# Optimization experiments

Hardware: AMD Instinct MI355X
Metric: run time of the kernel (lower is better)

## Reference

```python
import jax, jax.numpy as jnp
import numpy as np

H = 16          # num heads
HD = 88         # head dim = 1408 / 16
IMG = 336
PATCH = 14
THETA = 10000.0
IDX = IMG // PATCH          # 24 patches per side
SEQ = IDX * IDX + 1         # 576 patches + 1 CLS slot = 577


def _vision_rope_cos_sin():
    # Faithful to HF Llama4VisionRotaryEmbedding (rope_type='llama4', complex64):
    # 2D rope over (x, y) patch coordinates; CLS token gets zero rotation.
    img_idx = np.arange(IDX * IDX, dtype=np.int64).reshape(-1, 1)
    img_idx = np.concatenate([img_idx, img_idx[:1]], axis=0)
    img_idx[-1, -1] = -2  # CLS token marker
    fx = img_idx % IDX
    fy = img_idx // IDX
    freq_dim = HD // 2  # 44
    rope_freq = 1.0 / (THETA ** (np.arange(0, freq_dim, 2)[: freq_dim // 2].astype(np.float64) / freq_dim))
    freqs_x = np.repeat((fx + 1)[..., None] * rope_freq[None, None, :], 2, axis=-1)
    freqs_y = np.repeat((fy + 1)[..., None] * rope_freq[None, None, :], 2, axis=-1)
    freqs = np.concatenate([freqs_x, freqs_y], axis=-1)[..., ::2]  # [SEQ, 1, HD//2]
    freqs = np.where(img_idx.reshape(-1, 1, 1) < 0, 0.0, freqs)
    return jnp.asarray(np.cos(freqs), jnp.float32), jnp.asarray(np.sin(freqs), jnp.float32)


def _apply_rope(x, cos, sin):
    # x: [B, S, H, HD]; treat last dim as HD//2 complex pairs, rotate by e^{i*freq}
    xr = x.reshape(*x.shape[:-1], HD // 2, 2)
    a, b = xr[..., 0], xr[..., 1]               # [B, S, H, HD//2]
    out_r = a * cos - b * sin                   # cos/sin [S,1,HD//2] broadcast over B,H
    out_i = a * sin + b * cos
    return jnp.stack([out_r, out_i], axis=-1).reshape(x.shape)


def setup_inputs() -> dict:
    key = jax.random.key(0)
    ks = jax.random.split(key, 9)
    D = H * HD  # 1408
    B, S = 32, SEQ
    s = 0.02
    return {
        "hidden_states": jax.random.normal(ks[0], (B, S, D), jnp.float32),
        "wq": jax.random.normal(ks[1], (D, D), jnp.float32) * s,
        "bq": jax.random.normal(ks[2], (D,), jnp.float32) * s,
        "wk": jax.random.normal(ks[3], (D, D), jnp.float32) * s,
        "bk": jax.random.normal(ks[4], (D,), jnp.float32) * s,
        "wv": jax.random.normal(ks[5], (D, D), jnp.float32) * s,
        "bv": jax.random.normal(ks[6], (D,), jnp.float32) * s,
        "wo": jax.random.normal(ks[7], (D, D), jnp.float32) * s,
        "bo": jax.random.normal(ks[8], (D,), jnp.float32) * s,
    }


def reference(hidden_states, wq, bq, wk, bk, wv, bv, wo, bo):
    B, S, D = hidden_states.shape
    cos, sin = _vision_rope_cos_sin()
    # QKV projections (torch Linear convention: y = x @ W.T + b)
    q = (hidden_states @ wq.T + bq).reshape(B, S, H, HD)
    k = (hidden_states @ wk.T + bk).reshape(B, S, H, HD)
    v = (hidden_states @ wv.T + bv).reshape(B, S, H, HD)
    q = _apply_rope(q, cos, sin)
    k = _apply_rope(k, cos, sin)
    # Full (non-causal) self-attention
    scores = jnp.einsum('bqhd,bkhd->bhqk', q, k) * (HD ** -0.5)
    probs = jax.nn.softmax(scores, axis=-1)
    attn = jnp.einsum('bhqk,bkhd->bqhd', probs, v).reshape(B, S, D)
    return attn @ wo.T + bo
```

## Files before the change

kernel.cpp:

```cpp
#include <hip/hip_runtime.h>
#include <hip/hip_bf16.h>
#include <cstdint>
#include <cstddef>

#define NHEADS 16
#define HDIM   88
#define SEQLEN 577
#define NBATCH 32
#define DMODEL 1408
#define MROWS  (NBATCH * SEQLEN)
#define MTILES 145
#define MPAD   (MTILES * 128)
#define SP     592
#define SPT    592
#define DP     96
#define NFREQ  44
#define NBH    (NBATCH * NHEADS)

typedef __attribute__((ext_vector_type(8))) short short8;
typedef __attribute__((ext_vector_type(4))) float floatx4;

__device__ __forceinline__ unsigned short f2bf(float f) {
    union { float f; unsigned u; } v; v.f = f;
    unsigned u = v.u;
    u += 0x7fffu + ((u >> 16) & 1u);
    return (unsigned short)(u >> 16);
}

__device__ __forceinline__ void gload_lds16(const void* g, void* lds) {
    __builtin_amdgcn_global_load_lds(
        (__attribute__((address_space(1))) unsigned int*)g,
        (__attribute__((address_space(3))) unsigned int*)lds, 16, 0, 0);
}

__global__ void l4v_rope_table(float* __restrict__ cos_t, float* __restrict__ sin_t) {
    int idx = blockIdx.x * blockDim.x + threadIdx.x;
    if (idx >= SEQLEN * NFREQ) return;
    int s = idx / NFREQ, j = idx % NFREQ;
    float ang = 0.0f;
    if (s != SEQLEN - 1) {
        int coord = (j < 22) ? (s % 24) : (s / 24);
        int i = (j < 22) ? j : j - 22;
        float rf = __expf(-(2.0f * (float)i / 44.0f) * 9.21034037197618f);
        ang = (float)(coord + 1) * rf;
    }
    cos_t[idx] = cosf(ang);
    sin_t[idx] = sinf(ang);
}

__global__ void l4v_cvt_bf16(const float* __restrict__ in, unsigned short* __restrict__ out, int n) {
    int i = (blockIdx.x * blockDim.x + threadIdx.x) * 4;
    if (i + 3 < n) {
        float4 f = *(const float4*)(in + i);
        ushort4 o;
        o.x = f2bf(f.x); o.y = f2bf(f.y); o.z = f2bf(f.z); o.w = f2bf(f.w);
        *(ushort4*)(out + i) = o;
    } else {
        for (; i < n; i++) out[i] = f2bf(in[i]);
    }
}

__global__ __launch_bounds__(256, 3)
void l4v_gemm_qkv(const unsigned short* __restrict__ A,
                  const unsigned short* __restrict__ Wq,
                  const unsigned short* __restrict__ Wk,
                  const unsigned short* __restrict__ Wv,
                  const float* __restrict__ Bq,
                  const float* __restrict__ Bk,
                  const float* __restrict__ Bv,
                  const float* __restrict__ cos_t,
                  const float* __restrict__ sin_t,
                  unsigned short* __restrict__ Oq,
                  unsigned short* __restrict__ Ok,
                  unsigned short* __restrict__ OvT)
{
    __shared__ __align__(16) unsigned short a_sm[128 * 32];
    __shared__ __align__(16) unsigned short b_sm[128 * 32];

    const int tid  = threadIdx.x;
    const int lane = tid & 63;
    const int w    = tid >> 6;
    const int quad = lane >> 4;
    const int c    = lane & 15;
    const int wr   = w >> 1;
    const int wc   = w & 1;
    const int sel  = blockIdx.x % 3;
    const int n0   = (blockIdx.x / 3) * 128;
    const int m0   = blockIdx.y * 128;

    const unsigned short* Bw = (sel == 0) ? Wq : (sel == 1) ? Wk : Wv;
    const float* bias        = (sel == 0) ? Bq : (sel == 1) ? Bk : Bv;

    floatx4 acc[4][4];
#pragma unroll
    for (int i = 0; i < 4; i++)
#pragma unroll
        for (int j = 0; j < 4; j++) acc[i][j] = (floatx4)0.0f;

    const int chunk0 = w * 128 + lane;
    const int chunk1 = w * 128 + 64 + lane;
    const int r0 = chunk0 >> 2, ch0 = chunk0 & 3;
    const int r1 = chunk1 >> 2, ch1 = chunk1 & 3;
    const unsigned short* Ab = A  + (size_t)m0 * DMODEL;
    const unsigned short* Bb = Bw + (size_t)n0 * DMODEL;

    for (int k0 = 0; k0 < DMODEL; k0 += 32) {
        gload_lds16(Ab + (size_t)r0 * DMODEL + k0 + ch0 * 8, a_sm + (w * 128) * 8);
        gload_lds16(Ab + (size_t)r1 * DMODEL + k0 + ch1 * 8, a_sm + (w * 128 + 64) * 8);
        gload_lds16(Bb + (size_t)r0 * DMODEL + k0 + ch0 * 8, b_sm + (w * 128) * 8);
        gload_lds16(Bb + (size_t)r1 * DMODEL + k0 + ch1 * 8, b_sm + (w * 128 + 64) * 8);
        __syncthreads();
        short8 af[4], bfr[4];
#pragma unroll
        for (int mt = 0; mt < 4; mt++)
            af[mt] = *(const short8*)(a_sm + (wr * 64 + mt * 16 + c) * 32 + quad * 8);
#pragma unroll
        for (int nt = 0; nt < 4; nt++)
            bfr[nt] = *(const short8*)(b_sm + (wc * 64 + nt * 16 + c) * 32 + quad * 8);
#pragma unroll
        for (int mt = 0; mt < 4; mt++)
#pragma unroll
            for (int nt = 0; nt < 4; nt++)
                acc[mt][nt] = __builtin_amdgcn_mfma_f32_16x16x32_bf16(af[mt], bfr[nt], acc[mt][nt], 0, 0, 0);
        __syncthreads();
    }

    if (sel < 2) {
        unsigned short* outp = (sel == 0) ? Oq : Ok;
#pragma unroll
        for (int mt = 0; mt < 4; mt++) {
            int mbase = m0 + wr * 64 + mt * 16 + quad * 4;
#pragma unroll
            for (int nt = 0; nt < 4; nt++) {
                int n = n0 + wc * 64 + nt * 16 + c;
                float bi = bias[n];
                int h = n / HDIM, d = n % HDIM, j = d >> 1;
#pragma unroll
                for (int r = 0; r < 4; r++) {
                    int m = mbase + r;
                    int b = m / SEQLEN;
                    int s = m - b * SEQLEN;
                    float v = acc[mt][nt][r] + bi;
                    float pv = __shfl_xor(v, 1);
                    float cs = cos_t[s * NFREQ + j];
                    float sn = sin_t[s * NFREQ + j];
                    float outv = ((d & 1) == 0) ? (v * cs - pv * sn) : (pv * sn + v * cs);
                    if (m < MROWS)
                        outp[((size_t)(b * NHEADS + h) * SP + s) * DP + d] = f2bf(outv);
                }
            }
        }
    } else {
#pragma unroll
        for (int mt = 0; mt < 4; mt++) {
            int mbase = m0 + wr * 64 + mt * 16 + quad * 4;
#pragma unroll
            for (int nt = 0; nt < 4; nt++) {
                int n = n0 + wc * 64 + nt * 16 + c;
                float bi = bias[n];
                int h = n / HDIM, d = n % HDIM;
#pragma unroll
                for (int r = 0; r < 4; r++) {
                    int m = mbase + r;
                    if (m < MROWS) {
                        int b = m / SEQLEN;
                        int s = m - b * SEQLEN;
                        OvT[((size_t)((b * NHEADS + h) * DP + d)) * SPT + s] =
                            f2bf(acc[mt][nt][r] + bi);
                    }
                }
            }
        }
    }
}

__global__ __launch_bounds__(256, 3)
void l4v_gemm_out(const unsigned short* __restrict__ A,
                  const unsigned short* __restrict__ Bw,
                  const float* __restrict__ bias,
                  float* __restrict__ out_f32)
{
    __shared__ __align__(16) unsigned short a_sm[128 * 32];
    __shared__ __align__(16) unsigned short b_sm[128 * 32];

    const int tid  = threadIdx.x;
    const int lane = tid & 63;
    const int w    = tid >> 6;
    const int quad = lane >> 4;
    const int c    = lane & 15;
    const int wr   = w >> 1;
    const int wc   = w & 1;
    const int m0   = blockIdx.y * 128;
    const int n0   = blockIdx.x * 128;

    floatx4 acc[4][4];
#pragma unroll
    for (int i = 0; i < 4; i++)
#pragma unroll
        for (int j = 0; j < 4; j++) acc[i][j] = (floatx4)0.0f;

    const int chunk0 = w * 128 + lane;
    const int chunk1 = w * 128 + 64 + lane;
    const int r0 = chunk0 >> 2, ch0 = chunk0 & 3;
    const int r1 = chunk1 >> 2, ch1 = chunk1 & 3;
    const unsigned short* Ab = A  + (size_t)m0 * DMODEL;
    const unsigned short* Bb = Bw + (size_t)n0 * DMODEL;

    for (int k0 = 0; k0 < DMODEL; k0 += 32) {
        gload_lds16(Ab + (size_t)r0 * DMODEL + k0 + ch0 * 8, a_sm + (w * 128) * 8);
        gload_lds16(Ab + (size_t)r1 * DMODEL + k0 + ch1 * 8, a_sm + (w * 128 + 64) * 8);
        gload_lds16(Bb + (size_t)r0 * DMODEL + k0 + ch0 * 8, b_sm + (w * 128) * 8);
        gload_lds16(Bb + (size_t)r1 * DMODEL + k0 + ch1 * 8, b_sm + (w * 128 + 64) * 8);
        __syncthreads();
        short8 af[4], bfr[4];
#pragma unroll
        for (int mt = 0; mt < 4; mt++)
            af[mt] = *(const short8*)(a_sm + (wr * 64 + mt * 16 + c) * 32 + quad * 8);
#pragma unroll
        for (int nt = 0; nt < 4; nt++)
            bfr[nt] = *(const short8*)(b_sm + (wc * 64 + nt * 16 + c) * 32 + quad * 8);
#pragma unroll
        for (int mt = 0; mt < 4; mt++)
#pragma unroll
            for (int nt = 0; nt < 4; nt++)
                acc[mt][nt] = __builtin_amdgcn_mfma_f32_16x16x32_bf16(af[mt], bfr[nt], acc[mt][nt], 0, 0, 0);
        __syncthreads();
    }

#pragma unroll
    for (int mt = 0; mt < 4; mt++) {
        int mbase = m0 + wr * 64 + mt * 16 + quad * 4;
#pragma unroll
        for (int nt = 0; nt < 4; nt++) {
            int n = n0 + wc * 64 + nt * 16 + c;
            float bi = bias[n];
#pragma unroll
            for (int r = 0; r < 4; r++) {
                int m = mbase + r;
                if (m < MROWS) out_f32[(size_t)m * DMODEL + n] = acc[mt][nt][r] + bi;
            }
        }
    }
}

__global__ __launch_bounds__(256, 4)
void l4v_attn(const unsigned short* __restrict__ Q,
              const unsigned short* __restrict__ K,
              const unsigned short* __restrict__ VT,
              unsigned short* __restrict__ Obuf)
{
    __shared__ __align__(16) unsigned short k_sm[64 * 104];
    __shared__ __align__(16) unsigned short v_sm[96 * 72];
    __shared__ __align__(16) unsigned short p_sm[4][16 * 72];

    const int tid  = threadIdx.x;
    const int lane = tid & 63;
    const int w    = tid >> 6;
    const int quad = lane >> 4;
    const int c    = lane & 15;
    const int bh   = blockIdx.y;
    const int b    = bh >> 4, h = bh & 15;
    const size_t base  = (size_t)bh * SP * DP;
    const size_t baseT = (size_t)bh * DP * SPT;
    const float sl2e = 0.10660035817780522f * 1.4426950408889634f;

    for (int qi = 0; qi < 5; qi++) {
        const int qt = blockIdx.x * 5 + qi;

        int qrow = qt * 64 + w * 16 + c;
        if (qrow > SP - 1) qrow = SP - 1;
        short8 aq[3];
#pragma unroll
        for (int ks = 0; ks < 3; ks++)
            aq[ks] = *(const short8*)(Q + base + (size_t)qrow * DP + ks * 32 + quad * 8);

        float m_run[4], l_run[4];
        floatx4 o_acc[6];
#pragma unroll
        for (int r = 0; r < 4; r++) { m_run[r] = -INFINITY; l_run[r] = 0.0f; }
#pragma unroll
        for (int i = 0; i < 6; i++) o_acc[i] = (floatx4)0.0f;

        for (int kt = 0; kt < 10; kt++) {
#pragma unroll
            for (int i = 0; i < 3; i++) {
                int cc = tid + i * 256;
                int krr = cc / 12, kcol = cc - krr * 12;
                int krow = kt * 64 + krr;
                if (krow > SP - 1) krow = SP - 1;
                float4 kd = *(const float4*)(K + base + (size_t)krow * DP + kcol * 8);
                *(float4*)(k_sm + krr * 104 + kcol * 8) = kd;

                int vrow = cc >> 3, vcol = cc & 7;
                int scol = kt * 64 + vcol * 8;
                if (scol > SPT - 8) scol = SPT - 8;
                float4 vd = *(const float4*)(VT + baseT + (size_t)vrow * SPT + scol);
                *(float4*)(v_sm + vrow * 72 + vcol * 8) = vd;
            }
            __syncthreads();

            floatx4 sc[4];
#pragma unroll
            for (int nt = 0; nt < 4; nt++) {
                sc[nt] = (floatx4)0.0f;
#pragma unroll
                for (int ks = 0; ks < 3; ks++) {
                    short8 bk = *(const short8*)(k_sm + (nt * 16 + c) * 104 + ks * 32 + quad * 8);
                    sc[nt] = __builtin_amdgcn_mfma_f32_16x16x32_bf16(aq[ks], bk, sc[nt], 0, 0, 0);
                }
            }

            float t[4][4];
#pragma unroll
            for (int nt = 0; nt < 4; nt++) {
                int skcol = kt * 64 + nt * 16 + c;
                bool valid = (skcol < SEQLEN);
#pragma unroll
                for (int r = 0; r < 4; r++)
                    t[nt][r] = valid ? sc[nt][r] * sl2e : -INFINITY;
            }

            float mnew[4], alpha[4];
#pragma unroll
            for (int r = 0; r < 4; r++) {
                float v = fmaxf(fmaxf(t[0][r], t[1][r]), fmaxf(t[2][r], t[3][r]));
#pragma unroll
                for (int off = 1; off < 16; off <<= 1) v = fmaxf(v, __shfl_xor(v, off));
                mnew[r] = fmaxf(m_run[r], v);
                alpha[r] = exp2f(m_run[r] - mnew[r]);
                m_run[r] = mnew[r];
            }

            float p[4][4];
#pragma unroll
            for (int nt = 0; nt < 4; nt++)
#pragma unroll
                for (int r = 0; r < 4; r++)
                    p[nt][r] = exp2f(t[nt][r] - mnew[r]);

#pragma unroll
            for (int r = 0; r < 4; r++) {
                float sm = p[0][r] + p[1][r] + p[2][r] + p[3][r];
#pragma unroll
                for (int off = 1; off < 16; off <<= 1) sm += __shfl_xor(sm, off);
                l_run[r] = l_run[r] * alpha[r] + sm;
            }

#pragma unroll
            for (int nt = 0; nt < 4; nt++)
#pragma unroll
                for (int r = 0; r < 4; r++)
                    p_sm[w][(quad * 4 + r) * 72 + nt * 16 + c] = f2bf(p[nt][r]);

#pragma unroll
            for (int i = 0; i < 6; i++)
#pragma unroll
                for (int r = 0; r < 4; r++)
                    o_acc[i][r] *= alpha[r];

#pragma unroll
            for (int kp = 0; kp < 2; kp++) {
                short8 ap = *(const short8*)(&p_sm[w][c * 72 + kp * 32 + quad * 8]);
#pragma unroll
                for (int d2 = 0; d2 < 6; d2++) {
                    short8 bv = *(const short8*)(v_sm + (d2 * 16 + c) * 72 + kp * 32 + quad * 8);
                    o_acc[d2] = __builtin_amdgcn_mfma_f32_16x16x32_bf16(ap, bv, o_acc[d2], 0, 0, 0);
                }
            }
            __syncthreads();
        }

#pragma unroll
        for (int r = 0; r < 4; r++) {
            int sq = qt * 64 + w * 16 + quad * 4 + r;
            float il = 1.0f / l_run[r];
            if (sq < SEQLEN) {
                size_t rowoff = ((size_t)b * SEQLEN + sq) * DMODEL + h * HDIM;
#pragma unroll
                for (int d2 = 0; d2 < 6; d2++) {
                    int d = d2 * 16 + c;
                    if (d < HDIM) Obuf[rowoff + d] = f2bf(o_acc[d2][r] * il);
                }
            }
        }
    }
}

extern "C" void kernel_launch(void* const* d_in, const int* in_sizes, int n_in,
                              void* d_out, int out_size, void* d_ws, size_t ws_size,
                              hipStream_t stream)
{
    const float* hs = (const float*)d_in[0];
    const float* wq = (const float*)d_in[1];
    const float* bq = (const float*)d_in[2];
    const float* wk = (const float*)d_in[3];
    const float* bk = (const float*)d_in[4];
    const float* wv = (const float*)d_in[5];
    const float* bv = (const float*)d_in[6];
    const float* wo = (const float*)d_in[7];
    const float* bo = (const float*)d_in[8];
    float* out = (float*)d_out;

    char* ws = (char*)d_ws;
    size_t off = 0;
    auto alloc = [&](size_t bytes) -> char* {
        char* p = ws + off;
        off += (bytes + 255) & ~(size_t)255;
        return p;
    };

    unsigned short* hs_bf = (unsigned short*)alloc((size_t)MPAD * DMODEL * 2);
    unsigned short* wq_bf = (unsigned short*)alloc((size_t)DMODEL * DMODEL * 2);
    unsigned short* wk_bf = (unsigned short*)alloc((size_t)DMODEL * DMODEL * 2);
    unsigned short* wv_bf = (unsigned short*)alloc((size_t)DMODEL * DMODEL * 2);
    unsigned short* wo_bf = (unsigned short*)alloc((size_t)DMODEL * DMODEL * 2);
    unsigned short* qb    = (unsigned short*)alloc((size_t)NBH * SP * DP * 2);
    unsigned short* kb    = (unsigned short*)alloc((size_t)NBH * SP * DP * 2);
    unsigned short* vt    = (unsigned short*)alloc((size_t)NBH * DP * SPT * 2);
    float* cos_t = (float*)alloc((size_t)SEQLEN * NFREQ * 4);
    float* sin_t = (float*)alloc((size_t)SEQLEN * NFREQ * 4);
    unsigned short* attn_bf = hs_bf;

    if (off > ws_size) return;

    l4v_rope_table<<<dim3((SEQLEN * NFREQ + 255) / 256), dim3(256), 0, stream>>>(cos_t, sin_t);

    const int nhs = MROWS * DMODEL;
    l4v_cvt_bf16<<<dim3(nhs / 4 / 256), dim3(256), 0, stream>>>(hs, hs_bf, nhs);
    const int nw = DMODEL * DMODEL;
    l4v_cvt_bf16<<<dim3(nw / 4 / 256), dim3(256), 0, stream>>>(wq, wq_bf, nw);
    l4v_cvt_bf16<<<dim3(nw / 4 / 256), dim3(256), 0, stream>>>(wk, wk_bf, nw);
    l4v_cvt_bf16<<<dim3(nw / 4 / 256), dim3(256), 0, stream>>>(wv, wv_bf, nw);
    l4v_cvt_bf16<<<dim3(nw / 4 / 256), dim3(256), 0, stream>>>(wo, wo_bf, nw);

    l4v_gemm_qkv<<<dim3(33, MTILES), dim3(256), 0, stream>>>(
        hs_bf, wq_bf, wk_bf, wv_bf, bq, bk, bv, cos_t, sin_t, qb, kb, vt);

    l4v_attn<<<dim3(2, NBH), dim3(256), 0, stream>>>(qb, kb, vt, attn_bf);

    l4v_gemm_out<<<dim3(DMODEL / 128, MTILES), dim3(256), 0, stream>>>(attn_bf, wo_bf, bo, out);
}
```

Before: 1.043 ms.

## Double K-step per sync, swizzle GEMM block order, merge weight casts

Both GEMMs now load two 32-wide K slices into two LDS buffers per iteration, so each pair of barriers covers 64 K elements instead of 32. Blocks are launched on a 1D grid and remapped so groups of 29 M-tiles sweep all N-tiles together, which is meant to improve L2 reuse of the activation rows. The four weight bf16 conversions are merged into one launch. The change doubles LDS use per block, which may lower occupancy under launch_bounds(256,3). It also relies on MTILES=145 being exactly 5*29.

```diff
diff --git a/kernel.cpp b/kernel.cpp
--- a/kernel.cpp
+++ b/kernel.cpp
@@ -58,6 +58,22 @@
     } else {
         for (; i < n; i++) out[i] = f2bf(in[i]);
     }
+}
+
+__global__ void l4v_cvt_w4(const float* __restrict__ w0, const float* __restrict__ w1,
+                           const float* __restrict__ w2, const float* __restrict__ w3,
+                           unsigned short* __restrict__ o0, unsigned short* __restrict__ o1,
+                           unsigned short* __restrict__ o2, unsigned short* __restrict__ o3,
+                           int nw) {
+    int i = (blockIdx.x * blockDim.x + threadIdx.x) * 4;
+    int which = i / nw;
+    int local = i - which * nw;
+    const float* src = (which == 0) ? w0 : (which == 1) ? w1 : (which == 2) ? w2 : w3;
+    unsigned short* dst = (which == 0) ? o0 : (which == 1) ? o1 : (which == 2) ? o2 : o3;
+    float4 f = *(const float4*)(src + local);
+    ushort4 o;
+    o.x = f2bf(f.x); o.y = f2bf(f.y); o.z = f2bf(f.z); o.w = f2bf(f.w);
+    *(ushort4*)(dst + local) = o;
 }
 
 __global__ __launch_bounds__(256, 3)
@@ -74,8 +90,8 @@
                   unsigned short* __restrict__ Ok,
                   unsigned short* __restrict__ OvT)
 {
-    __shared__ __align__(16) unsigned short a_sm[128 * 32];
-    __shared__ __align__(16) unsigned short b_sm[128 * 32];
+    __shared__ __align__(16) unsigned short a_sm[2][128 * 32];
+    __shared__ __align__(16) unsigned short b_sm[2][128 * 32];
 
     const int tid  = threadIdx.x;
     const int lane = tid & 63;
@@ -84,9 +100,15 @@
     const int c    = lane & 15;
     const int wr   = w >> 1;
     const int wc   = w & 1;
-    const int sel  = blockIdx.x % 3;
-    const int n0   = (blockIdx.x / 3) * 128;
-    const int m0   = blockIdx.y * 128;
+
+    const int bid  = blockIdx.x;
+    const int SG   = 29 * 33;
+    const int sg   = bid / SG;
+    const int rr   = bid - sg * SG;
+    const int m0   = (sg * 29 + (rr % 29)) * 128;
+    const int xsel = rr / 29;
+    const int sel  = xsel / 11;
+    const int n0   = (xsel - sel * 11) * 128;
 
     const unsigned short* Bw = (sel == 0) ? Wq : (sel == 1) ? Wk : Wv;
     const float* bias        = (sel == 0) ? Bq : (sel == 1) ? Bk : Bv;
@@ -104,24 +126,33 @@
     const unsigned short* Ab = A  + (size_t)m0 * DMODEL;
     const unsigned short* Bb = Bw + (size_t)n0 * DMODEL;
 
-    for (int k0 = 0; k0 < DMODEL; k0 += 32) {
-        gload_lds16(Ab + (size_t)r0 * DMODEL + k0 + ch0 * 8, a_sm + (w * 128) * 8);
-        gload_lds16(Ab + (size_t)r1 * DMODEL + k0 + ch1 * 8, a_sm + (w * 128 + 64) * 8);
-        gload_lds16(Bb + (size_t)r0 * DMODEL + k0 + ch0 * 8, b_sm + (w * 128) * 8);
-        gload_lds16(Bb + (size_t)r1 * DMODEL + k0 + ch1 * 8, b_sm + (w * 128 + 64) * 8);
+    for (int k0 = 0; k0 < DMODEL; k0 += 64) {
+#pragma unroll
+        for (int p = 0; p < 2; p++) {
+            int kc = k0 + p * 32;
+            gload_lds16(Ab + (size_t)r0 * DMODEL + kc + ch0 * 8, a_sm[p] + (w * 128) * 8);
+            gload_lds16(Ab + (size_t)r1 * DMODEL + kc + ch1 * 8, a_sm[p] + (w * 128 + 64) * 8);
+            gload_lds16(Bb + (size_t)r0 * DMODEL + kc + ch0 * 8, b_sm[p] + (w * 128) * 8);
+            gload_lds16(Bb + (size_t)r1 * DMODEL + kc + ch1 * 8, b_sm[p] + (w * 128 + 64) * 8);
+        }
         __syncthreads();
-        short8 af[4], bfr[4];
-#pragma unroll
-        for (int mt = 0; mt < 4; mt++)
-            af[mt] = *(const short8*)(a_sm + (wr * 64 + mt * 16 + c) * 32 + quad * 8);
-#pragma unroll
-        for (int nt = 0; nt < 4; nt++)
-            bfr[nt] = *(const short8*)(b_sm + (wc * 64 + nt * 16 + c) * 32 + quad * 8);
-#pragma unroll
-        for (int mt = 0; mt < 4; mt++)
+        short8 af[2][4], bfr[2][4];
+#pragma unroll
+        for (int p = 0; p < 2; p++) {
+#pragma unroll
+            for (int mt = 0; mt < 4; mt++)
+                af[p][mt] = *(const short8*)(a_sm[p] + (wr * 64 + mt * 16 + c) * 32 + quad * 8);
 #pragma unroll
             for (int nt = 0; nt < 4; nt++)
-                acc[mt][nt] = __builtin_amdgcn_mfma_f32_16x16x32_bf16(af[mt], bfr[nt], acc[mt][nt], 0, 0, 0);
+                bfr[p][nt] = *(const short8*)(b_sm[p] + (wc * 64 + nt * 16 + c) * 32 + quad * 8);
+        }
+#pragma unroll
+        for (int p = 0; p < 2; p++)
+#pragma unroll
+            for (int mt = 0; mt < 4; mt++)
+#pragma unroll
+                for (int nt = 0; nt < 4; nt++)
+                    acc[mt][nt] = __builtin_amdgcn_mfma_f32_16x16x32_bf16(af[p][mt], bfr[p][nt], acc[mt][nt], 0, 0, 0);
         __syncthreads();
     }
 
@@ -180,8 +211,8 @@
                   const float* __restrict__ bias,
                   float* __restrict__ out_f32)
 {
-    __shared__ __align__(16) unsigned short a_sm[128 * 32];
-    __shared__ __align__(16) unsigned short b_sm[128 * 32];
+    __shared__ __align__(16) unsigned short a_sm[2][128 * 32];
+    __shared__ __align__(16) unsigned short b_sm[2][128 * 32];
 
     const int tid  = threadIdx.x;
     const int lane = tid & 63;
@@ -190,8 +221,13 @@
     const int c    = lane & 15;
     const int wr   = w >> 1;
     const int wc   = w & 1;
-    const int m0   = blockIdx.y * 128;
-    const int n0   = blockIdx.x * 128;
+
+    const int bid = blockIdx.x;
+    const int SG  = 29 * 11;
+    const int sg  = bid / SG;
+    const int rr  = bid - sg * SG;
+    const int m0  = (sg * 29 + (rr % 29)) * 128;
+    const int n0  = (rr / 29) * 128;
 
     floatx4 acc[4][4];
 #pragma unroll
@@ -206,24 +242,33 @@
     const unsigned short* Ab = A  + (size_t)m0 * DMODEL;
     const unsigned short* Bb = Bw + (size_t)n0 * DMODEL;
 
-    for (int k0 = 0; k0 < DMODEL; k0 += 32) {
-        gload_lds16(Ab + (size_t)r0 * DMODEL + k0 + ch0 * 8, a_sm + (w * 128) * 8);
-        gload_lds16(Ab + (size_t)r1 * DMODEL + k0 + ch1 * 8, a_sm + (w * 128 + 64) * 8);
-        gload_lds16(Bb + (size_t)r0 * DMODEL + k0 + ch0 * 8, b_sm + (w * 128) * 8);
-        gload_lds16(Bb + (size_t)r1 * DMODEL + k0 + ch1 * 8, b_sm + (w * 128 + 64) * 8);
+    for (int k0 = 0; k0 < DMODEL; k0 += 64) {
+#pragma unroll
+        for (int p = 0; p < 2; p++) {
+            int kc = k0 + p * 32;
+            gload_lds16(Ab + (size_t)r0 * DMODEL + kc + ch0 * 8, a_sm[p] + (w * 128) * 8);
+            gload_lds16(Ab + (size_t)r1 * DMODEL + kc + ch1 * 8, a_sm[p] + (w * 128 + 64) * 8);
+            gload_lds16(Bb + (size_t)r0 * DMODEL + kc + ch0 * 8, b_sm[p] + (w * 128) * 8);
+            gload_lds16(Bb + (size_t)r1 * DMODEL + kc + ch1 * 8, b_sm[p] + (w * 128 + 64) * 8);
+        }
         __syncthreads();
-        short8 af[4], bfr[4];
-#pragma unroll
-        for (int mt = 0; mt < 4; mt++)
-            af[mt] = *(const short8*)(a_sm + (wr * 64 + mt * 16 + c) * 32 + quad * 8);
-#pragma unroll
-        for (int nt = 0; nt < 4; nt++)
-            bfr[nt] = *(const short8*)(b_sm + (wc * 64 + nt * 16 + c) * 32 + quad * 8);
-#pragma unroll
-        for (int mt = 0; mt < 4; mt++)
+        short8 af[2][4], bfr[2][4];
+#pragma unroll
+        for (int p = 0; p < 2; p++) {
+#pragma unroll
+            for (int mt = 0; mt < 4; mt++)
+                af[p][mt] = *(const short8*)(a_sm[p] + (wr * 64 + mt * 16 + c) * 32 + quad * 8);
 #pragma unroll
             for (int nt = 0; nt < 4; nt++)
-                acc[mt][nt] = __builtin_amdgcn_mfma_f32_16x16x32_bf16(af[mt], bfr[nt], acc[mt][nt], 0, 0, 0);
+                bfr[p][nt] = *(const short8*)(b_sm[p] + (wc * 64 + nt * 16 + c) * 32 + quad * 8);
+        }
+#pragma unroll
+        for (int p = 0; p < 2; p++)
+#pragma unroll
+            for (int mt = 0; mt < 4; mt++)
+#pragma unroll
+                for (int nt = 0; nt < 4; nt++)
+                    acc[mt][nt] = __builtin_amdgcn_mfma_f32_16x16x32_bf16(af[p][mt], bfr[p][nt], acc[mt][nt], 0, 0, 0);
         __syncthreads();
     }
 
@@ -428,15 +473,13 @@
     const int nhs = MROWS * DMODEL;
     l4v_cvt_bf16<<<dim3(nhs / 4 / 256), dim3(256), 0, stream>>>(hs, hs_bf, nhs);
     const int nw = DMODEL * DMODEL;
-    l4v_cvt_bf16<<<dim3(nw / 4 / 256), dim3(256), 0, stream>>>(wq, wq_bf, nw);
-    l4v_cvt_bf16<<<dim3(nw / 4 / 256), dim3(256), 0, stream>>>(wk, wk_bf, nw);
-    l4v_cvt_bf16<<<dim3(nw / 4 / 256), dim3(256), 0, stream>>>(wv, wv_bf, nw);
-    l4v_cvt_bf16<<<dim3(nw / 4 / 256), dim3(256), 0, stream>>>(wo, wo_bf, nw);
-
-    l4v_gemm_qkv<<<dim3(33, MTILES), dim3(256), 0, stream>>>(
+    l4v_cvt_w4<<<dim3(nw / 256), dim3(256), 0, stream>>>(wq, wk, wv, wo,
+                                                         wq_bf, wk_bf, wv_bf, wo_bf, nw);
+
+    l4v_gemm_qkv<<<dim3(5 * 29 * 33), dim3(256), 0, stream>>>(
         hs_bf, wq_bf, wk_bf, wv_bf, bq, bk, bv, cos_t, sin_t, qb, kb, vt);
 
     l4v_attn<<<dim3(2, NBH), dim3(256), 0, stream>>>(qb, kb, vt, attn_bf);
 
-    l4v_gemm_out<<<dim3(DMODEL / 128, MTILES), dim3(256), 0, stream>>>(attn_bf, wo_bf, bo, out);
-}
+    l4v_gemm_out<<<dim3(5 * 29 * 11), dim3(256), 0, stream>>>(attn_bf, wo_bf, bo, out);
+}
```

Measured after the change: 1.050 ms. About the same (+0.6%).
